# Performance work log

Hardware: AMD Instinct MI355X
Metric: run time of the kernel (lower is better)

The kernel has to match this reference:

```python
import jax, jax.numpy as jnp
import numpy as np

B, T, WIN, CIN, H, COUT = 512, 64, 256, 4, 512, 2


def setup_inputs() -> dict:
    key = jax.random.key(0)
    k = jax.random.split(key, 4)
    D = WIN * CIN  # 1024
    s = 0.02
    return {
        "inputs": jax.random.normal(k[0], (B, T, WIN, CIN), dtype=jnp.float32),
        "W_in": jax.random.normal(k[1], (D, 3 * H), dtype=jnp.float32) * s,
        "b_in": jnp.zeros((3 * H,), dtype=jnp.float32),
        "U": jax.random.normal(k[2], (H, 3 * H), dtype=jnp.float32) * s,
        "b_rec": jnp.zeros((3 * H,), dtype=jnp.float32),
        "W2": jax.random.normal(k[3], (2 * H, WIN * COUT), dtype=jnp.float32) * s,
        "b2": jnp.zeros((WIN * COUT,), dtype=jnp.float32),
    }


def _gru_last_state(x, W_in, b_in, U, b_rec):
    # Keras GRU v2 math: reset_after=True, recurrent_activation=sigmoid,
    # activation=relu (as configured). training=False -> no dropout.
    Bm, Tm, _ = x.shape
    Hm = U.shape[0]
    # precompute input projections for all timesteps: [B, T, 3H]
    xg = jnp.einsum("btd,dh->bth", x, W_in) + b_in

    def step(h, xg_t):
        hg = h @ U + b_rec  # recurrent bias applied before reset gate (reset_after)
        xz, xr, xh = jnp.split(xg_t, 3, axis=-1)
        hz, hr, hh = jnp.split(hg, 3, axis=-1)
        z = jax.nn.sigmoid(xz + hz)
        r = jax.nn.sigmoid(xr + hr)
        h_cand = jax.nn.relu(xh + r * hh)
        h_new = z * h + (1.0 - z) * h_cand
        return h_new, None

    h0 = jnp.zeros((Bm, Hm), dtype=x.dtype)
    hT, _ = jax.lax.scan(step, h0, jnp.swapaxes(xg, 0, 1))
    return hT  # [B, H]; with return_sequences=False, output == final_state


def reference(inputs, W_in, b_in, U, b_rec, W2, b2):
    Bm, Tm = inputs.shape[0], inputs.shape[1]
    x = inputs.reshape(Bm, Tm, -1)  # flatten window*channels -> [B, T, 1024]
    hT = _gru_last_state(x, W_in, b_in, U, b_rec)
    cat = jnp.concatenate([hT, hT], axis=-1)  # tf.concat((output, final_state))
    out = cat @ W2 + b2
    return out.reshape(Bm, WIN, COUT)
```

## Files before the change

### kernel.cpp

```cpp
#include <hip/hip_runtime.h>
#include <hip/hip_bf16.h>
#include <stdint.h>

#define BATCH 512
#define TSTEPS 64
#define DIN 1024
#define HID 512
#define G3 1536
#define MROWS (BATCH * TSTEPS)
#define POUT 512

typedef __attribute__((ext_vector_type(8))) short bf16x8;
typedef __attribute__((ext_vector_type(4))) float f32x4;

__device__ __forceinline__ float bf2f(short s) {
  union { unsigned u; float f; } v;
  v.u = ((unsigned)(unsigned short)s) << 16;
  return v.f;
}
__device__ __forceinline__ short f2bf(float f) {
  __hip_bfloat16 h = __float2bfloat16(f);
  short s;
  __builtin_memcpy(&s, &h, 2);
  return s;
}
__device__ __forceinline__ void gload_lds16(const void* g, void* l) {
  __builtin_amdgcn_global_load_lds(
      (const __attribute__((address_space(1))) void*)g,
      (__attribute__((address_space(3))) void*)l, 16, 0, 0);
}

__global__ __launch_bounds__(256) void xcast(const float* __restrict__ in,
                                             short* __restrict__ out) {
  const size_t i = ((size_t)blockIdx.x * 256 + threadIdx.x) * 8;
  const float4 a = *reinterpret_cast<const float4*>(in + i);
  const float4 b = *reinterpret_cast<const float4*>(in + i + 4);
  bf16x8 v;
  v[0] = f2bf(a.x); v[1] = f2bf(a.y); v[2] = f2bf(a.z); v[3] = f2bf(a.w);
  v[4] = f2bf(b.x); v[5] = f2bf(b.y); v[6] = f2bf(b.z); v[7] = f2bf(b.w);
  *reinterpret_cast<bf16x8*>(out + i) = v;
}

__global__ __launch_bounds__(256) void transpose_cast(const float* __restrict__ in,
                                                      short* __restrict__ out,
                                                      int R, int C) {
  __shared__ float tile[32][33];
  const int c0 = blockIdx.x * 32, r0 = blockIdx.y * 32;
  const int tx = threadIdx.x & 31, ty = threadIdx.x >> 5;
#pragma unroll
  for (int i = 0; i < 4; ++i) {
    const int r = r0 + ty + i * 8;
    tile[ty + i * 8][tx] = in[(size_t)r * C + c0 + tx];
  }
  __syncthreads();
#pragma unroll
  for (int i = 0; i < 4; ++i) {
    const int c = c0 + ty + i * 8;
    out[(size_t)c * R + r0 + tx] = f2bf(tile[tx][ty + i * 8]);
  }
}

__global__ __launch_bounds__(256) void u_pack2(const float* __restrict__ U,
                                               short* __restrict__ Upk2) {
  const unsigned idx = blockIdx.x * 256 + threadIdx.x;
  const unsigned e = idx & 7u;
  unsigned tmp = idx >> 3;
  const unsigned lc = tmp & 15u; tmp >>= 4;
  const unsigned lg = tmp & 3u;  tmp >>= 2;
  const unsigned wn = tmp & 3u;  tmp >>= 2;
  const unsigned f = tmp % 48u;
  const unsigned cg = tmp / 48u;
  const unsigned g = f >> 4, kc = f & 15u;
  const unsigned k = kc * 32u + lg * 8u + e;
  const unsigned col = g * 512u + cg * 64u + wn * 16u + lc;
  Upk2[idx] = f2bf(U[(size_t)k * G3 + col]);
}

__global__ __launch_bounds__(256) void gemm_xg_mfma(const short* __restrict__ Xbf,
                                                    const short* __restrict__ Wt,
                                                    const float* __restrict__ bin,
                                                    __hip_bfloat16* __restrict__ XG) {
  __shared__ __align__(16) short As[128 * 64];
  __shared__ __align__(16) short Bs[128 * 64];
  const int tid = threadIdx.x;
  const int w = tid >> 6, l = tid & 63;
  const int lc = l & 15, lg = l >> 4;

  const int xcd = blockIdx.x & 7;
  const int idx = blockIdx.x >> 3;
  const int wg = xcd * 384 + idx;
  const int rt = wg / 12, ct = wg % 12;
  const int row0 = rt * 128, col0 = ct * 128;

  const int wm = w >> 1, wn = w & 1;

  f32x4 acc[4][4];
#pragma unroll
  for (int mt = 0; mt < 4; ++mt)
#pragma unroll
    for (int nt = 0; nt < 4; ++nt) acc[mt][nt] = (f32x4){0.f, 0.f, 0.f, 0.f};

  for (int k0 = 0; k0 < DIN; k0 += 64) {
    __syncthreads();
#pragma unroll
    for (int i = 0; i < 4; ++i) {
      const int rr = w * 32 + i * 8 + (l >> 3);
      const int s = (l & 7) ^ (rr & 7);
      gload_lds16(&Xbf[(size_t)(row0 + rr) * DIN + k0 + s * 8],
                  (char*)As + (w * 32 + i * 8) * 128);
      gload_lds16(&Wt[(size_t)(col0 + rr) * DIN + k0 + s * 8],
                  (char*)Bs + (w * 32 + i * 8) * 128);
    }
    __syncthreads();
#pragma unroll
    for (int kc = 0; kc < 2; ++kc) {
      bf16x8 a[4], b[4];
#pragma unroll
      for (int mt = 0; mt < 4; ++mt) {
        const int R = wm * 64 + mt * 16 + lc;
        const int ch = (kc * 4 + lg) ^ (R & 7);
        a[mt] = *reinterpret_cast<const bf16x8*>((const char*)As + R * 128 + ch * 16);
      }
#pragma unroll
      for (int nt = 0; nt < 4; ++nt) {
        const int Rn = wn * 64 + nt * 16 + lc;
        const int ch = (kc * 4 + lg) ^ (Rn & 7);
        b[nt] = *reinterpret_cast<const bf16x8*>((const char*)Bs + Rn * 128 + ch * 16);
      }
#pragma unroll
      for (int mt = 0; mt < 4; ++mt)
#pragma unroll
        for (int nt = 0; nt < 4; ++nt)
          acc[mt][nt] = __builtin_amdgcn_mfma_f32_16x16x32_bf16(a[mt], b[nt],
                                                                acc[mt][nt], 0, 0, 0);
    }
  }

  float bv[4];
#pragma unroll
  for (int nt = 0; nt < 4; ++nt) bv[nt] = bin[col0 + wn * 64 + nt * 16 + lc];
#pragma unroll
  for (int mt = 0; mt < 4; ++mt) {
#pragma unroll
    for (int nt = 0; nt < 4; ++nt) {
      const int col = col0 + wn * 64 + nt * 16 + lc;
      const int g = col >> 9;
      const int rem = col & 511;
      const int cgc = rem >> 6, cc = rem & 63;
#pragma unroll
      for (int rr = 0; rr < 4; ++rr) {
        const int m = row0 + wm * 64 + mt * 16 + lg * 4 + rr;
        const int t = m & 63, b = m >> 6;
        const size_t o =
            ((((size_t)t * 16 + (b >> 5)) * 8 + cgc) * 32 + (b & 31)) * 192 +
            g * 64 + cc;
        XG[o] = __float2bfloat16(acc[mt][nt][rr] + bv[nt]);
      }
    }
  }
}

__global__ __launch_bounds__(512, 2) void gru_scan_coop(
    const __hip_bfloat16* __restrict__ XG, const short* __restrict__ Upk2,
    const float* __restrict__ brec, short* h_g, unsigned* bar,
    float* __restrict__ HT) {
  __shared__ __align__(16) short hS[32 * 512];
  __shared__ __align__(16) short xgL[2][6144];
  const int tid = threadIdx.x, w = tid >> 6, l = tid & 63;
  const int lc = l & 15, lg = l >> 4;
  const int bg = blockIdx.x >> 3, cgi = blockIdx.x & 7;
  const int b0 = bg * 32, c0 = cgi * 64;
  const int wm = w & 1, wn = w >> 1;
  unsigned* const flags = bar + bg * 16;

  bf16x8 ub[3][16];
#pragma unroll
  for (int g = 0; g < 3; ++g)
#pragma unroll
    for (int kc = 0; kc < 16; ++kc)
      ub[g][kc] = *reinterpret_cast<const bf16x8*>(
          Upk2 + ((((size_t)cgi * 48 + g * 16 + kc) * 4 + wn) * 4 + lg) * 128 +
          lc * 8);

  for (int i = tid; i < 4096; i += 512) ((unsigned long long*)hS)[i] = 0ull;

  const short* XGs = (const short*)XG;
  {
    const short* xs = XGs + ((size_t)bg * 8 + cgi) * 6144;
    gload_lds16(xs + tid * 8, (char*)xgL[0] + w * 1024);
    if (tid < 256)
      gload_lds16(xs + (512 + tid) * 8, (char*)xgL[0] + 8192 + w * 1024);
  }

  const int j = c0 + wn * 16 + lc;
  const float brz = brec[j], brr = brec[512 + j], brh = brec[1024 + j];
  const int arow = wm * 16 + lc;

  __syncthreads();

  for (int t = 0; t < TSTEPS; ++t) {
    f32x4 za0 = (f32x4){0.f, 0.f, 0.f, 0.f}, za1 = za0, za2 = za0;
    if (t > 0) {
      for (;;) {
        const unsigned f = __hip_atomic_load(&flags[l & 7], __ATOMIC_RELAXED,
                                             __HIP_MEMORY_SCOPE_AGENT);
        if (__all((int)(f >= (unsigned)t))) break;
        __builtin_amdgcn_s_sleep(1);
      }
      const unsigned long long* hsrc = (const unsigned long long*)(
          h_g + ((size_t)(t & 1) * BATCH + b0) * 512);
      unsigned long long v[8];
#pragma unroll
      for (int r = 0; r < 8; ++r)
        v[r] = __hip_atomic_load(hsrc + r * 512 + tid, __ATOMIC_RELAXED,
                                 __HIP_MEMORY_SCOPE_AGENT);
#pragma unroll
      for (int r = 0; r < 8; ++r)
        ((unsigned long long*)hS)[r * 512 + tid] = v[r];
      __syncthreads();

#pragma unroll
      for (int kc = 0; kc < 16; ++kc) {
        const int s = kc * 4 + lg;
        const bf16x8 a = *(const bf16x8*)((const char*)hS + arow * 1024 +
                                          ((s ^ (arow & 7)) << 4));
        za0 = __builtin_amdgcn_mfma_f32_16x16x32_bf16(a, ub[0][kc], za0, 0, 0, 0);
        za1 = __builtin_amdgcn_mfma_f32_16x16x32_bf16(a, ub[1][kc], za1, 0, 0, 0);
        za2 = __builtin_amdgcn_mfma_f32_16x16x32_bf16(a, ub[2][kc], za2, 0, 0, 0);
      }
    }

    const short* xb = xgL[t & 1];
#pragma unroll
    for (int r = 0; r < 4; ++r) {
      const int lb = wm * 16 + lg * 4 + r;
      const float xz = bf2f(xb[lb * 192 + wn * 16 + lc]);
      const float xr = bf2f(xb[lb * 192 + 64 + wn * 16 + lc]);
      const float xh = bf2f(xb[lb * 192 + 128 + wn * 16 + lc]);
      const float z = 1.f / (1.f + __expf(-(xz + za0[r] + brz)));
      const float rg = 1.f / (1.f + __expf(-(xr + za1[r] + brr)));
      const float hc = fmaxf(fmaf(rg, za2[r] + brh, xh), 0.f);
      const int hoff = lb * 1024 + (((j >> 3) ^ (lb & 7)) << 4) + (j & 7) * 2;
      const float hold = bf2f(*(const short*)((const char*)hS + hoff));
      const float hnew = fmaf(z, hold - hc, hc);
      if (t == TSTEPS - 1) {
        HT[(size_t)(b0 + lb) * HID + j] = hnew;
      } else {
        __hip_atomic_store(
            (unsigned short*)((char*)h_g +
                              ((size_t)((t + 1) & 1) * BATCH + b0) * 1024 + hoff),
            (unsigned short)f2bf(hnew), __ATOMIC_RELAXED,
            __HIP_MEMORY_SCOPE_AGENT);
      }
    }
    if (t == TSTEPS - 1) break;

    __syncthreads();
    if (tid == 0)
      __hip_atomic_store(&flags[cgi], (unsigned)(t + 1), __ATOMIC_RELAXED,
                         __HIP_MEMORY_SCOPE_AGENT);
    {
      const short* xs = XGs + (((size_t)(t + 1) * 16 + bg) * 8 + cgi) * 6144;
      char* xd = (char*)xgL[(t + 1) & 1];
      gload_lds16(xs + tid * 8, xd + w * 1024);
      if (tid < 256)
        gload_lds16(xs + (512 + tid) * 8, xd + 8192 + w * 1024);
    }
  }
}

__global__ __launch_bounds__(256) void final_proj(const float* __restrict__ HT,
                                                  const float* __restrict__ W2,
                                                  const float* __restrict__ b2,
                                                  float* __restrict__ OUT) {
  const int b = blockIdx.x >> 1;
  const int pp = ((blockIdx.x & 1) << 8) + threadIdx.x;
  float acc = b2[pp];
  const float* h = &HT[(size_t)b * HID];
  for (int k = 0; k < HID; ++k)
    acc = fmaf(h[k], W2[(size_t)k * POUT + pp] + W2[(size_t)(k + HID) * POUT + pp], acc);
  OUT[(size_t)b * POUT + pp] = acc;
}

extern "C" void kernel_launch(void* const* d_in, const int* in_sizes, int n_in,
                              void* d_out, int out_size, void* d_ws,
                              size_t ws_size, hipStream_t stream) {
  const float* X    = (const float*)d_in[0];
  const float* Win  = (const float*)d_in[1];
  const float* bin  = (const float*)d_in[2];
  const float* U    = (const float*)d_in[3];
  const float* brec = (const float*)d_in[4];
  const float* W2   = (const float*)d_in[5];
  const float* b2   = (const float*)d_in[6];
  float* OUT = (float*)d_out;

  char* ws = (char*)d_ws;
  size_t off = 0;
  __hip_bfloat16* XG = (__hip_bfloat16*)(ws + off); off += (size_t)MROWS * G3 * 2;
  short* Wt   = (short*)(ws + off); off += (size_t)G3 * DIN * 2;
  short* Upk2 = (short*)(ws + off); off += (size_t)G3 * HID * 2;
  float* HT   = (float*)(ws + off); off += (size_t)BATCH * HID * 4;
  short* h_g  = (short*)(ws + off); off += (size_t)2 * BATCH * HID * 2;
  unsigned* bar = (unsigned*)(ws + off); off += 4096;
  short* Xbf  = (short*)(ws + off); off += (size_t)MROWS * DIN * 2;

  hipMemsetAsync(bar, 0, 1024, stream);

  xcast<<<(MROWS * DIN) / (256 * 8), 256, 0, stream>>>(X, Xbf);
  transpose_cast<<<dim3(G3 / 32, DIN / 32), 256, 0, stream>>>(Win, Wt, DIN, G3);
  u_pack2<<<(HID * G3) / 256, 256, 0, stream>>>(U, Upk2);
  gemm_xg_mfma<<<(MROWS / 128) * (G3 / 128), 256, 0, stream>>>(Xbf, Wt, bin, XG);

  const __hip_bfloat16* XGc = XG;
  const short* Upkc = Upk2;
  void* args[] = {(void*)&XGc, (void*)&Upkc, (void*)&brec,
                  (void*)&h_g, (void*)&bar, (void*)&HT};
  hipLaunchCooperativeKernel((const void*)gru_scan_coop, dim3(128), dim3(512),
                             args, 0, stream);

  final_proj<<<(BATCH * POUT) / 256, 256, 0, stream>>>(HT, W2, b2, OUT);
}
```

Baseline: 464.6 us.

## Replace scalar final projection with bf16 MFMA GEMM and prefolded W2

The final projection now folds the two halves of W2 (since the concatenated input is [hT,hT]) into one transposed bf16 matrix in a pre-pass, and the scan writes the last hidden state as bf16. A tiled MFMA GEMM kernel with swizzled LDS staging then replaces the scalar per-output dot-product kernel. This removes the strided fp32 W2 reads and scalar FMAs, but adds an extra pack kernel launch, bf16 rounding of hT and W2, and uses only 16 blocks.

```diff
diff --git a/kernel.cpp b/kernel.cpp
--- a/kernel.cpp
+++ b/kernel.cpp
@@ -57,6 +57,25 @@
   for (int i = 0; i < 4; ++i) {
     const int c = c0 + ty + i * 8;
     out[(size_t)c * R + r0 + tx] = f2bf(tile[tx][ty + i * 8]);
+  }
+}
+
+__global__ __launch_bounds__(256) void w2_pack(const float* __restrict__ W2,
+                                               short* __restrict__ W2st) {
+  __shared__ float tile[32][33];
+  const int c0 = blockIdx.x * 32, r0 = blockIdx.y * 32;
+  const int tx = threadIdx.x & 31, ty = threadIdx.x >> 5;
+#pragma unroll
+  for (int i = 0; i < 4; ++i) {
+    const int r = r0 + ty + i * 8;
+    tile[ty + i * 8][tx] = W2[(size_t)r * POUT + c0 + tx] +
+                           W2[(size_t)(r + HID) * POUT + c0 + tx];
+  }
+  __syncthreads();
+#pragma unroll
+  for (int i = 0; i < 4; ++i) {
+    const int c = c0 + ty + i * 8;
+    W2st[(size_t)c * HID + r0 + tx] = f2bf(tile[tx][ty + i * 8]);
   }
 }
 
@@ -163,7 +182,7 @@
 __global__ __launch_bounds__(512, 2) void gru_scan_coop(
     const __hip_bfloat16* __restrict__ XG, const short* __restrict__ Upk2,
     const float* __restrict__ brec, short* h_g, unsigned* bar,
-    float* __restrict__ HT) {
+    short* __restrict__ HTb) {
   __shared__ __align__(16) short hS[32 * 512];
   __shared__ __align__(16) short xgL[2][6144];
   const int tid = threadIdx.x, w = tid >> 6, l = tid & 63;
@@ -244,7 +263,7 @@
       const float hold = bf2f(*(const short*)((const char*)hS + hoff));
       const float hnew = fmaf(z, hold - hc, hc);
       if (t == TSTEPS - 1) {
-        HT[(size_t)(b0 + lb) * HID + j] = hnew;
+        HTb[(size_t)(b0 + lb) * HID + j] = f2bf(hnew);
       } else {
         __hip_atomic_store(
             (unsigned short*)((char*)h_g +
@@ -269,17 +288,75 @@
   }
 }
 
-__global__ __launch_bounds__(256) void final_proj(const float* __restrict__ HT,
-                                                  const float* __restrict__ W2,
+__global__ __launch_bounds__(256) void final_mfma(const short* __restrict__ HTb,
+                                                  const short* __restrict__ W2st,
                                                   const float* __restrict__ b2,
                                                   float* __restrict__ OUT) {
-  const int b = blockIdx.x >> 1;
-  const int pp = ((blockIdx.x & 1) << 8) + threadIdx.x;
-  float acc = b2[pp];
-  const float* h = &HT[(size_t)b * HID];
-  for (int k = 0; k < HID; ++k)
-    acc = fmaf(h[k], W2[(size_t)k * POUT + pp] + W2[(size_t)(k + HID) * POUT + pp], acc);
-  OUT[(size_t)b * POUT + pp] = acc;
+  __shared__ __align__(16) short As[128 * 64];
+  __shared__ __align__(16) short Bs[128 * 64];
+  const int tid = threadIdx.x;
+  const int w = tid >> 6, l = tid & 63;
+  const int lc = l & 15, lg = l >> 4;
+  const int row0 = (blockIdx.x >> 2) * 128, col0 = (blockIdx.x & 3) * 128;
+  const int wm = w >> 1, wn = w & 1;
+
+  f32x4 acc[4][4];
+#pragma unroll
+  for (int mt = 0; mt < 4; ++mt)
+#pragma unroll
+    for (int nt = 0; nt < 4; ++nt) acc[mt][nt] = (f32x4){0.f, 0.f, 0.f, 0.f};
+
+  for (int k0 = 0; k0 < HID; k0 += 64) {
+    __syncthreads();
+#pragma unroll
+    for (int i = 0; i < 4; ++i) {
+      const int rr = w * 32 + i * 8 + (l >> 3);
+      const int s = (l & 7) ^ (rr & 7);
+      gload_lds16(&HTb[(size_t)(row0 + rr) * HID + k0 + s * 8],
+                  (char*)As + (w * 32 + i * 8) * 128);
+      gload_lds16(&W2st[(size_t)(col0 + rr) * HID + k0 + s * 8],
+                  (char*)Bs + (w * 32 + i * 8) * 128);
+    }
+    __syncthreads();
+#pragma unroll
+    for (int kc = 0; kc < 2; ++kc) {
+      bf16x8 a[4], b[4];
+#pragma unroll
+      for (int mt = 0; mt < 4; ++mt) {
+        const int R = wm * 64 + mt * 16 + lc;
+        const int ch = (kc * 4 + lg) ^ (R & 7);
+        a[mt] = *reinterpret_cast<const bf16x8*>((const char*)As + R * 128 + ch * 16);
+      }
+#pragma unroll
+      for (int nt = 0; nt < 4; ++nt) {
+        const int Rn = wn * 64 + nt * 16 + lc;
+        const int ch = (kc * 4 + lg) ^ (Rn & 7);
+        b[nt] = *reinterpret_cast<const bf16x8*>((const char*)Bs + Rn * 128 + ch * 16);
+      }
+#pragma unroll
+      for (int mt = 0; mt < 4; ++mt)
+#pragma unroll
+        for (int nt = 0; nt < 4; ++nt)
+          acc[mt][nt] = __builtin_amdgcn_mfma_f32_16x16x32_bf16(a[mt], b[nt],
+                                                                acc[mt][nt], 0, 0, 0);
+    }
+  }
+
+  float bv[4];
+#pragma unroll
+  for (int nt = 0; nt < 4; ++nt) bv[nt] = b2[col0 + wn * 64 + nt * 16 + lc];
+#pragma unroll
+  for (int mt = 0; mt < 4; ++mt) {
+#pragma unroll
+    for (int nt = 0; nt < 4; ++nt) {
+      const int col = col0 + wn * 64 + nt * 16 + lc;
+#pragma unroll
+      for (int rr = 0; rr < 4; ++rr) {
+        const int row = row0 + wm * 64 + mt * 16 + lg * 4 + rr;
+        OUT[(size_t)row * POUT + col] = acc[mt][nt][rr] + bv[nt];
+      }
+    }
+  }
 }
 
 extern "C" void kernel_launch(void* const* d_in, const int* in_sizes, int n_in,
@@ -299,7 +376,8 @@
   __hip_bfloat16* XG = (__hip_bfloat16*)(ws + off); off += (size_t)MROWS * G3 * 2;
   short* Wt   = (short*)(ws + off); off += (size_t)G3 * DIN * 2;
   short* Upk2 = (short*)(ws + off); off += (size_t)G3 * HID * 2;
-  float* HT   = (float*)(ws + off); off += (size_t)BATCH * HID * 4;
+  short* HTb  = (short*)(ws + off); off += (size_t)BATCH * HID * 2;
+  short* W2st = (short*)(ws + off); off += (size_t)HID * POUT * 2;
   short* h_g  = (short*)(ws + off); off += (size_t)2 * BATCH * HID * 2;
   unsigned* bar = (unsigned*)(ws + off); off += 4096;
   short* Xbf  = (short*)(ws + off); off += (size_t)MROWS * DIN * 2;
@@ -309,14 +387,15 @@
   xcast<<<(MROWS * DIN) / (256 * 8), 256, 0, stream>>>(X, Xbf);
   transpose_cast<<<dim3(G3 / 32, DIN / 32), 256, 0, stream>>>(Win, Wt, DIN, G3);
   u_pack2<<<(HID * G3) / 256, 256, 0, stream>>>(U, Upk2);
+  w2_pack<<<dim3(POUT / 32, HID / 32), 256, 0, stream>>>(W2, W2st);
   gemm_xg_mfma<<<(MROWS / 128) * (G3 / 128), 256, 0, stream>>>(Xbf, Wt, bin, XG);
 
   const __hip_bfloat16* XGc = XG;
   const short* Upkc = Upk2;
   void* args[] = {(void*)&XGc, (void*)&Upkc, (void*)&brec,
-                  (void*)&h_g, (void*)&bar, (void*)&HT};
+                  (void*)&h_g, (void*)&bar, (void*)&HTb};
   hipLaunchCooperativeKernel((const void*)gru_scan_coop, dim3(128), dim3(512),
                              args, 0, stream);
 
-  final_proj<<<(BATCH * POUT) / 256, 256, 0, stream>>>(HT, W2, b2, OUT);
-}
+  final_mfma<<<16, 256, 0, stream>>>(HTb, W2st, b2, OUT);
+}
```

After: 430.1 us. 1.08x faster.
